# Performance work log

Hardware: AMD Instinct MI355X
Metric: run time of the kernel (lower is better)

Reference implementation:

```python
import jax, jax.numpy as jnp
import numpy as np


def _position_table(seq_len, d_model, dtype):
    # position[i, j] = sin(i / 10000**((j+1)/d))  if j even
    #                  cos(i / 10000**((j+1)/d))  if j odd
    # (note the nonstandard (j+1)/d exponent, faithful to the source)
    i = jnp.arange(seq_len, dtype=dtype)[:, None]          # [S, 1]
    j = jnp.arange(d_model, dtype=dtype)[None, :]          # [1, D]
    pf = i / jnp.power(jnp.asarray(10000.0, dtype), (j + 1.0) / d_model)  # [S, D]
    even = (jnp.arange(d_model) % 2 == 0)[None, :]
    return jnp.where(even, jnp.sin(pf), jnp.cos(pf))       # [S, D]


def setup_inputs() -> dict:
    key = jax.random.key(0)
    x = jax.random.normal(key, (4, 8192, 1024), dtype=jnp.float32)
    return {"x": x}


def reference(x) -> jnp.ndarray:
    B, S, D = x.shape
    pos = _position_table(S, D, x.dtype)
    return x + pos[None, :, :]
```

## Files before the change

### kernel.cpp

```cpp
#include <hip/hip_runtime.h>
#include <math.h>

#define PE_S 8192
#define PE_D 1024
#define PE_B 4

typedef float f32x4 __attribute__((ext_vector_type(4)));

__device__ __forceinline__ float pe_sin(float fs, float wrev) {
    float t = fs * wrev;
    float r = t - floorf(t);
    r += fmaf(fs, wrev, -t);
    return __builtin_amdgcn_sinf(r);
}
__device__ __forceinline__ float pe_cos(float fs, float wrev) {
    float t = fs * wrev;
    float r = t - floorf(t);
    r += fmaf(fs, wrev, -t);
    return __builtin_amdgcn_cosf(r);
}

__global__ __launch_bounds__(256) void position_encoder_kernel(
    const float* __restrict__ x, float* __restrict__ out) {
    const int tid = blockIdx.x * blockDim.x + threadIdx.x;
    const int d4  = tid & (PE_D / 4 - 1);
    const int s   = (tid >> 8) & (PE_S - 1);
    const int d0  = d4 << 2;

    const float fs = (float)s;
    const float A2 = -0.012976281620653760f;
    const float C  = -2.6514961294723187f;

    const float w0 = exp2f(fmaf((float)(d0 + 1), A2, C));
    const float w1 = exp2f(fmaf((float)(d0 + 2), A2, C));
    const float w2 = exp2f(fmaf((float)(d0 + 3), A2, C));
    const float w3 = exp2f(fmaf((float)(d0 + 4), A2, C));

    const size_t off = (size_t)tid * 4;
    const f32x4 v = *reinterpret_cast<const f32x4*>(x + off);

    f32x4 o;
    o.x = v.x + pe_sin(fs, w0);
    o.y = v.y + pe_cos(fs, w1);
    o.z = v.z + pe_sin(fs, w2);
    o.w = v.w + pe_cos(fs, w3);
    *reinterpret_cast<f32x4*>(out + off) = o;
}

extern "C" void kernel_launch(void* const* d_in, const int* in_sizes, int n_in,
                              void* d_out, int out_size, void* d_ws, size_t ws_size,
                              hipStream_t stream) {
    const float* x = (const float*)d_in[0];
    float* out = (float*)d_out;

    const int threads = 256;
    const int total_quads = PE_B * PE_S * PE_D / 4;
    const int blocks = total_quads / threads;
    position_encoder_kernel<<<blocks, threads, 0, stream>>>(x, out);
}
```

Measured before the change: 218.7 us.

## Grid-stride loop reusing position encodings across batch pairs

Switches to a fixed grid of 2048 blocks where each thread loops eight times and processes two batch entries per iteration that share the same sequence position. The per-column frequency weights are computed once per thread, and the sin/cos values are shared across the two batch elements, roughly halving transcendental work. The trade-off is fewer resident blocks, which relies on the unrolled loads for memory parallelism.

```diff
diff --git a/kernel.cpp b/kernel.cpp
--- a/kernel.cpp
+++ b/kernel.cpp
@@ -4,6 +4,12 @@
 #define PE_S 8192
 #define PE_D 1024
 #define PE_B 4
+
+#define PE_BLOCKS 2048
+#define PE_THREADS 256
+#define PE_HALFQ (PE_B * PE_S * PE_D / 4 / 2)
+#define PE_STRIDE (PE_BLOCKS * PE_THREADS)
+#define PE_ITERS (PE_HALFQ / PE_STRIDE)
 
 typedef float f32x4 __attribute__((ext_vector_type(4)));
 
@@ -20,31 +26,40 @@
     return __builtin_amdgcn_cosf(r);
 }
 
-__global__ __launch_bounds__(256) void position_encoder_kernel(
+__global__ __launch_bounds__(PE_THREADS) void position_encoder_kernel(
     const float* __restrict__ x, float* __restrict__ out) {
-    const int tid = blockIdx.x * blockDim.x + threadIdx.x;
-    const int d4  = tid & (PE_D / 4 - 1);
-    const int s   = (tid >> 8) & (PE_S - 1);
-    const int d0  = d4 << 2;
+    const int tid0 = blockIdx.x * blockDim.x + threadIdx.x;
+    const int d0   = (tid0 & (PE_D / 4 - 1)) << 2;
 
-    const float fs = (float)s;
     const float A2 = -0.012976281620653760f;
     const float C  = -2.6514961294723187f;
-
     const float w0 = exp2f(fmaf((float)(d0 + 1), A2, C));
     const float w1 = exp2f(fmaf((float)(d0 + 2), A2, C));
     const float w2 = exp2f(fmaf((float)(d0 + 3), A2, C));
     const float w3 = exp2f(fmaf((float)(d0 + 4), A2, C));
 
-    const size_t off = (size_t)tid * 4;
-    const f32x4 v = *reinterpret_cast<const f32x4*>(x + off);
+#pragma unroll
+    for (int it = 0; it < PE_ITERS; ++it) {
+        const int q   = tid0 + it * PE_STRIDE;
+        const int row = q >> 8;
+        const int s   = row & (PE_S - 1);
 
-    f32x4 o;
-    o.x = v.x + pe_sin(fs, w0);
-    o.y = v.y + pe_cos(fs, w1);
-    o.z = v.z + pe_sin(fs, w2);
-    o.w = v.w + pe_cos(fs, w3);
-    *reinterpret_cast<f32x4*>(out + off) = o;
+        const size_t offA = (size_t)q * 4;
+        const size_t offB = (size_t)(q + PE_HALFQ) * 4;
+
+        const f32x4 va = *reinterpret_cast<const f32x4*>(x + offA);
+        const f32x4 vb = *reinterpret_cast<const f32x4*>(x + offB);
+
+        const float fs = (float)s;
+        f32x4 p;
+        p.x = pe_sin(fs, w0);
+        p.y = pe_cos(fs, w1);
+        p.z = pe_sin(fs, w2);
+        p.w = pe_cos(fs, w3);
+
+        *reinterpret_cast<f32x4*>(out + offA) = va + p;
+        *reinterpret_cast<f32x4*>(out + offB) = vb + p;
+    }
 }
 
 extern "C" void kernel_launch(void* const* d_in, const int* in_sizes, int n_in,
@@ -52,9 +67,5 @@
                               hipStream_t stream) {
     const float* x = (const float*)d_in[0];
     float* out = (float*)d_out;
-
-    const int threads = 256;
-    const int total_quads = PE_B * PE_S * PE_D / 4;
-    const int blocks = total_quads / threads;
-    position_encoder_kernel<<<blocks, threads, 0, stream>>>(x, out);
+    position_encoder_kernel<<<PE_BLOCKS, PE_THREADS, 0, stream>>>(x, out);
 }
```

Result: slower. 233.2 us (+6.6%).

## Reuse position encoding across batch and use nontemporal loads/stores

Applied to the files above, without the earlier changes.

Each thread now computes the sin/cos position values once and applies them to all four batch planes, so the grid shrinks by the batch factor. The four batch loads are issued up front to increase memory-level parallelism, and loads and stores use nontemporal hints to avoid polluting the cache. Fewer blocks may reduce latency hiding, but the kernel is bandwidth bound over 256MB of traffic, so the main gain is cutting the transcendental work by four.

```diff
diff --git a/kernel.cpp b/kernel.cpp
--- a/kernel.cpp
+++ b/kernel.cpp
@@ -23,28 +23,39 @@
 __global__ __launch_bounds__(256) void position_encoder_kernel(
     const float* __restrict__ x, float* __restrict__ out) {
     const int tid = blockIdx.x * blockDim.x + threadIdx.x;
-    const int d4  = tid & (PE_D / 4 - 1);
-    const int s   = (tid >> 8) & (PE_S - 1);
-    const int d0  = d4 << 2;
+    const int d0  = (tid & (PE_D / 4 - 1)) << 2;
+    const int s   = tid >> 8;
 
-    const float fs = (float)s;
+    const size_t base  = (size_t)tid * 4;
+    const size_t plane = (size_t)PE_S * PE_D;
+
+    const f32x4 v0 = __builtin_nontemporal_load(
+        reinterpret_cast<const f32x4*>(x + 0 * plane + base));
+    const f32x4 v1 = __builtin_nontemporal_load(
+        reinterpret_cast<const f32x4*>(x + 1 * plane + base));
+    const f32x4 v2 = __builtin_nontemporal_load(
+        reinterpret_cast<const f32x4*>(x + 2 * plane + base));
+    const f32x4 v3 = __builtin_nontemporal_load(
+        reinterpret_cast<const f32x4*>(x + 3 * plane + base));
+
     const float A2 = -0.012976281620653760f;
     const float C  = -2.6514961294723187f;
-
     const float w0 = exp2f(fmaf((float)(d0 + 1), A2, C));
     const float w1 = exp2f(fmaf((float)(d0 + 2), A2, C));
     const float w2 = exp2f(fmaf((float)(d0 + 3), A2, C));
     const float w3 = exp2f(fmaf((float)(d0 + 4), A2, C));
 
-    const size_t off = (size_t)tid * 4;
-    const f32x4 v = *reinterpret_cast<const f32x4*>(x + off);
+    const float fs = (float)s;
+    f32x4 p;
+    p.x = pe_sin(fs, w0);
+    p.y = pe_cos(fs, w1);
+    p.z = pe_sin(fs, w2);
+    p.w = pe_cos(fs, w3);
 
-    f32x4 o;
-    o.x = v.x + pe_sin(fs, w0);
-    o.y = v.y + pe_cos(fs, w1);
-    o.z = v.z + pe_sin(fs, w2);
-    o.w = v.w + pe_cos(fs, w3);
-    *reinterpret_cast<f32x4*>(out + off) = o;
+    __builtin_nontemporal_store(v0 + p, reinterpret_cast<f32x4*>(out + 0 * plane + base));
+    __builtin_nontemporal_store(v1 + p, reinterpret_cast<f32x4*>(out + 1 * plane + base));
+    __builtin_nontemporal_store(v2 + p, reinterpret_cast<f32x4*>(out + 2 * plane + base));
+    __builtin_nontemporal_store(v3 + p, reinterpret_cast<f32x4*>(out + 3 * plane + base));
 }
 
 extern "C" void kernel_launch(void* const* d_in, const int* in_sizes, int n_in,
@@ -54,7 +65,7 @@
     float* out = (float*)d_out;
 
     const int threads = 256;
-    const int total_quads = PE_B * PE_S * PE_D / 4;
+    const int total_quads = PE_S * PE_D / 4;
     const int blocks = total_quads / threads;
     position_encoder_kernel<<<blocks, threads, 0, stream>>>(x, out);
 }
```

Result: slower. 224.9 us (+2.9%).
